# Optimization experiments

Measured on AMD Instinct MI355X. Metric: run time of the kernel, lower is better.

The kernel has to match this reference:

```python
import jax, jax.numpy as jnp
import numpy as np

N, E, D, DFF, OUT = 50000, 800000, 128, 256, 119
NUM_MASK = 7500

def setup_inputs() -> dict:
    key = jax.random.key(0)
    ks = jax.random.split(key, 12)
    return {
        "x": jax.random.normal(ks[0], (N, D), jnp.float32),
        "edge_index": jax.random.randint(ks[1], (2, E), 0, N, jnp.int64),
        "edge_attr": jax.random.randint(ks[2], (E, 2), 0, 3, jnp.int64),
        "masked_idx": jax.random.randint(ks[3], (NUM_MASK,), 0, N, jnp.int64),
        "prelu_a": jnp.float32(0.25),
        "W_enc": jax.random.normal(ks[4], (D, D), jnp.float32) * (1.0 / np.sqrt(D)),
        "emb1": jax.random.normal(ks[5], (6, D), jnp.float32) * 0.1,
        "emb2": jax.random.normal(ks[6], (3, D), jnp.float32) * 0.1,
        "W1": jax.random.normal(ks[7], (DFF, D), jnp.float32) * (1.0 / np.sqrt(D)),
        "b1": jnp.zeros((DFF,), jnp.float32),
        "W2": jax.random.normal(ks[8], (OUT, DFF), jnp.float32) * (1.0 / np.sqrt(DFF)),
        "b2": jnp.zeros((OUT,), jnp.float32),
    }

def reference(x, edge_index, edge_attr, masked_idx, prelu_a, W_enc, emb1, emb2, W1, b1, W2, b2):
    n = x.shape[0]
    # PReLU -> enc_to_dec (no bias) -> zero masked nodes
    h = jnp.where(x > 0, x, prelu_a * x)
    h = h @ W_enc.T
    h = h.at[masked_idx].set(0.0)
    # add self loops (self-loop edge_attr = [4, 0])
    loop = jnp.arange(n, dtype=edge_index.dtype)
    src = jnp.concatenate([edge_index[0], loop])
    dst = jnp.concatenate([edge_index[1], loop])
    et = jnp.concatenate([edge_attr[:, 0], jnp.full((n,), 4, edge_attr.dtype)])
    ed = jnp.concatenate([edge_attr[:, 1], jnp.zeros((n,), edge_attr.dtype)])
    edge_emb = emb1[et] + emb2[ed]          # [E+N, D]
    msg = h[src] + edge_emb                 # gather + add
    aggr = jax.ops.segment_sum(msg, dst, num_segments=n)  # scatter-add
    # GIN MLP update
    hid = jax.nn.relu(aggr @ W1.T + b1)
    return hid @ W2.T + b2
```

## Files before the change

kernel.cpp:

```cpp
#include <hip/hip_runtime.h>
#include <hip/hip_fp16.h>


typedef unsigned long long ull;
typedef _Float16 half8 __attribute__((ext_vector_type(8)));
typedef float    f32x4 __attribute__((ext_vector_type(4)));

#define MFMA16(a, b, c) __builtin_amdgcn_mfma_f32_16x16x32_f16(a, b, c, 0, 0, 0)
#define BCAP 4608
#define EPB  2048

__global__ __launch_bounds__(256) void k_wconv(const float* __restrict__ Wen,
                                               const float* __restrict__ W1,
                                               const float* __restrict__ W2,
                                               const float* __restrict__ b1,
                                               const float* __restrict__ emb1,
                                               const float* __restrict__ emb2,
                                               __half* __restrict__ Wc16,
                                               __half* __restrict__ W2_16p,
                                               float* __restrict__ tabs,
                                               int* __restrict__ gcur,
                                               int* __restrict__ off,
                                               int n, int E)
{
    int b = blockIdx.x, t = threadIdx.x;
    if (b < 128) {
        __shared__ float We[128 * 128];
        for (int i = t; i < 4096; i += 256) {
            int j = i >> 5, k4 = (i & 31) << 2;
            *(float4*)(We + (j << 7) + k4) = *(const float4*)(Wen + (j << 7) + k4);
        }
        __syncthreads();
        int r = (b << 1) | (t >> 7);
        int k = t & 127;
        const float* w1r = W1 + ((size_t)r << 7);
        float acc = 0.f;
#pragma unroll 8
        for (int j = 0; j < 128; ++j)
            acc = fmaf(w1r[j], We[(j << 7) + k], acc);
        Wc16[(r << 7) + k] = __float2half(acc);
    } else if (b < 192) {
#pragma unroll
        for (int u = 0; u < 2; ++u) {
            int i = (b - 128) * 512 + u * 256 + t;
            int r = i >> 8;
            W2_16p[i] = (r < 119) ? __float2half(W2[i]) : __half(0.0f);
        }
    } else if (b == 192) {
        int col = t;
        const float* w1r = W1 + ((size_t)col << 7);
        float s = 0.f, t0 = 0.f, t1 = 0.f, t2 = 0.f,
              u0 = 0.f, u1 = 0.f, u2 = 0.f;
        for (int j = 0; j < 128; ++j) {
            float w = w1r[j];
            s  = fmaf(emb1[512 + j] + emb2[j], w, s);
            t0 = fmaf(emb1[j],        w, t0);
            t1 = fmaf(emb1[128 + j],  w, t1);
            t2 = fmaf(emb1[256 + j],  w, t2);
            u0 = fmaf(emb2[j],        w, u0);
            u1 = fmaf(emb2[128 + j],  w, u1);
            u2 = fmaf(emb2[256 + j],  w, u2);
        }
        tabs[col]            = s + b1[col];
        tabs[256 + col]      = t0;
        tabs[512 + col]      = t1;
        tabs[768 + col]      = t2;
        tabs[1024 + col]     = u0;
        tabs[1280 + col]     = u1;
        tabs[1536 + col]     = u2;
    } else {
        gcur[t] = 0;
        if (t == 0) off[n] = E;
    }
}

__global__ __launch_bounds__(256) void k_pre(const float* __restrict__ x,
                                             const float* __restrict__ prelu_a,
                                             uint2* __restrict__ px16u2,
                                             const int* __restrict__ ei,
                                             const int* __restrict__ ea,
                                             int* __restrict__ gcur,
                                             unsigned int* __restrict__ binned,
                                             int n, int E, int nbPx, int nbBin)
{
    __shared__ int lcnt[256];
    int t = threadIdx.x;

    if ((int)blockIdx.x >= nbPx) {
        int b = blockIdx.x - nbPx;
        int e0 = b * EPB;
        lcnt[t] = 0;
        __syncthreads();
        unsigned int rec[8];
        int bk[8];
#pragma unroll
        for (int u = 0; u < 8; ++u) {
            int e = e0 + u * 256 + t;
            if (e < E) {
                int src = ei[e];
                int dst = ei[E + e];
                int et  = ea[2 * e];
                int ed  = ea[2 * e + 1];
                rec[u] = (unsigned int)src | ((unsigned int)et << 17)
                       | ((unsigned int)ed << 19)
                       | ((unsigned int)(dst & 255) << 21);
                bk[u] = dst >> 8;
                atomicAdd(&lcnt[bk[u]], 1);
            } else bk[u] = -1;
        }
        __syncthreads();
        int c = lcnt[t];
        lcnt[t] = (c > 0) ? atomicAdd(&gcur[t], c) : 0;
        __syncthreads();
#pragma unroll
        for (int u = 0; u < 8; ++u) {
            if (bk[u] >= 0) {
                int pos = atomicAdd(&lcnt[bk[u]], 1);
                if (pos < BCAP) binned[(size_t)bk[u] * BCAP + pos] = rec[u];
            }
        }
        return;
    }

    int idx = blockIdx.x * 256 + t;
    if (idx < n * 32) {
        float a = prelu_a[0];
        float4 v = *(const float4*)((const float*)x + (size_t)idx * 4);
        v.x = v.x > 0.f ? v.x : a * v.x;
        v.y = v.y > 0.f ? v.y : a * v.y;
        v.z = v.z > 0.f ? v.z : a * v.z;
        v.w = v.w > 0.f ? v.w : a * v.w;
        __half2 lo = __floats2half2_rn(v.x, v.y);
        __half2 hi = __floats2half2_rn(v.z, v.w);
        uint2 o;
        o.x = *(unsigned int*)&lo;
        o.y = *(unsigned int*)&hi;
        px16u2[idx] = o;
    }
}

__global__ void k_mask(const int* __restrict__ midx,
                       unsigned int* __restrict__ px16u, int nm)
{
    int idx = blockIdx.x * blockDim.x + threadIdx.x;
    if (idx >= nm * 64) return;
    int m = idx >> 6, l = idx & 63;
    px16u[(((size_t)midx[m]) << 6) + l] = 0u;
}

__global__ __launch_bounds__(256) void k_bucket(const unsigned int* __restrict__ binned,
                                                const int* __restrict__ gcur,
                                                ull* __restrict__ cnt64,
                                                int* __restrict__ off,
                                                int* __restrict__ sorted,
                                                int n, int nb)
{
    __shared__ ull lc[256];
    __shared__ int sg[2][256];
    __shared__ int curs[256];
    int b = blockIdx.x >> 1, half = blockIdx.x & 1;
    int t = threadIdx.x;

    int gv = (t < nb) ? min(gcur[t], BCAP) : 0;
    sg[0][t] = gv;
    lc[t] = 0;
    __syncthreads();
    int cb = 0;
    for (int d = 1; d < 256; d <<= 1) {
        int v = sg[cb][t];
        if (t >= d) v += sg[cb][t - d];
        sg[cb ^ 1][t] = v;
        cb ^= 1;
        __syncthreads();
    }
    int ebase = (b == 0) ? 0 : sg[cb][b - 1];
    int mcnt = min(gcur[b], BCAP);
    __syncthreads();

    const unsigned int* bp = binned + (size_t)b * BCAP;
    for (int i = t; i < mcnt; i += 256) {
        unsigned int rec = bp[i];
        int dl = (rec >> 21) & 255;
        int et = (rec >> 17) & 3;
        int ed = (rec >> 19) & 3;
        atomicAdd(&lc[dl], (1ULL << (10 * et)) | (1ULL << (30 + 10 * ed)));
    }
    __syncthreads();

    ull c = lc[t];
    int deg = (int)((c & 1023) + ((c >> 10) & 1023) + ((c >> 20) & 1023));
    sg[0][t] = deg;
    __syncthreads();
    cb = 0;
    for (int d = 1; d < 256; d <<= 1) {
        int v = sg[cb][t];
        if (t >= d) v += sg[cb][t - d];
        sg[cb ^ 1][t] = v;
        cb ^= 1;
        __syncthreads();
    }
    int loc = sg[cb][t] - deg;
    int dst = (b << 8) + t;
    if (dst < n && (t >> 7) == half) {
        cnt64[dst] = c;
        off[dst]   = ebase + loc;
    }
    curs[t] = ebase + loc;
    __syncthreads();

    for (int i = t; i < mcnt; i += 256) {
        unsigned int rec = bp[i];
        int dl = (rec >> 21) & 255;
        if ((dl >> 7) != half) continue;
        int p = atomicAdd(&curs[dl], 1);
        sorted[p] = (int)(rec & 0x1FFFF);
    }
}

__global__ __launch_bounds__(256) void k_agg(const uint2* __restrict__ px2,
                                             const int* __restrict__ off,
                                             const int* __restrict__ sorted,
                                             uint2* __restrict__ agg2, int n)
{
    int t = threadIdx.x;
    int l32 = t & 31;
    int node = blockIdx.x * 8 + (t >> 5);
    if (node >= n) return;

    uint2 hv = px2[(size_t)node * 32 + l32];
    float2 hA = __half22float2(*(__half2*)&hv.x);
    float2 hB = __half22float2(*(__half2*)&hv.y);
    float4 base = make_float4(hA.x, hA.y, hB.x, hB.y);

    __half2 aL[4], aH[4];
#pragma unroll
    for (int u = 0; u < 4; ++u) { aL[u] = __half2(); aH[u] = __half2(); }
    int i = off[node], e = off[node + 1];
    for (; i + 3 < e; i += 4) {
        int s0 = sorted[i],     s1 = sorted[i + 1];
        int s2 = sorted[i + 2], s3 = sorted[i + 3];
        uint2 v0 = px2[(size_t)s0 * 32 + l32];
        uint2 v1 = px2[(size_t)s1 * 32 + l32];
        uint2 v2 = px2[(size_t)s2 * 32 + l32];
        uint2 v3 = px2[(size_t)s3 * 32 + l32];
        aL[0] = __hadd2(aL[0], *(__half2*)&v0.x);
        aH[0] = __hadd2(aH[0], *(__half2*)&v0.y);
        aL[1] = __hadd2(aL[1], *(__half2*)&v1.x);
        aH[1] = __hadd2(aH[1], *(__half2*)&v1.y);
        aL[2] = __hadd2(aL[2], *(__half2*)&v2.x);
        aH[2] = __hadd2(aH[2], *(__half2*)&v2.y);
        aL[3] = __hadd2(aL[3], *(__half2*)&v3.x);
        aH[3] = __hadd2(aH[3], *(__half2*)&v3.y);
    }
    for (; i < e; ++i) {
        uint2 v0 = px2[(size_t)sorted[i] * 32 + l32];
        aL[0] = __hadd2(aL[0], *(__half2*)&v0.x);
        aH[0] = __hadd2(aH[0], *(__half2*)&v0.y);
    }
#pragma unroll
    for (int u = 0; u < 4; ++u) {
        float2 fL = __half22float2(aL[u]);
        float2 fH = __half22float2(aH[u]);
        base.x += fL.x; base.y += fL.y;
        base.z += fH.x; base.w += fH.y;
    }
    __half2 oL = __floats2half2_rn(base.x, base.y);
    __half2 oH = __floats2half2_rn(base.z, base.w);
    uint2 o;
    o.x = *(unsigned int*)&oL;
    o.y = *(unsigned int*)&oH;
    agg2[(size_t)node * 32 + l32] = o;
}

__global__ __launch_bounds__(256, 2) void k_mlp1(const __half* __restrict__ agg16,
                                                 const __half* __restrict__ Wc16,
                                                 const float* __restrict__ tabs,
                                                 const ull* __restrict__ cnt64,
                                                 __half* __restrict__ hid16, int n)
{
    __shared__ __half Wl[256 * 136];
    __shared__ float tl[7 * 256];
    int t = threadIdx.x;
    for (int c = t; c < 4096; c += 256) {
        int row = c >> 4, slot = c & 15;
        *(uint4*)((char*)Wl + row * 272 + slot * 16) =
            *(const uint4*)((const char*)Wc16 + (size_t)c * 16);
    }
    for (int c = t; c < 1792; c += 256) tl[c] = tabs[c];
    __syncthreads();
    int lane = t & 63, wid = t >> 6;
    int rowbase = blockIdx.x * 128 + wid * 32;
    int mr0 = min(rowbase + (lane & 15), n - 1);
    int mr1 = min(rowbase + 16 + (lane & 15), n - 1);
    int kg = (lane >> 4) * 8, slotb = lane >> 4;
    f32x4 acc[32] = {};
#pragma unroll
    for (int ks = 0; ks < 4; ++ks) {
        half8 a0 = *(const half8*)(agg16 + ((size_t)mr0 << 7) + ks * 32 + kg);
        half8 a1 = *(const half8*)(agg16 + ((size_t)mr1 << 7) + ks * 32 + kg);
        const char* wp = (const char*)Wl + (size_t)(lane & 15) * 272
                       + (ks * 4 + slotb) * 16;
#pragma unroll
        for (int ct = 0; ct < 16; ++ct) {
            half8 bf = *(const half8*)(wp + ct * (16 * 272));
            acc[ct * 2]     = MFMA16(a0, bf, acc[ct * 2]);
            acc[ct * 2 + 1] = MFMA16(a1, bf, acc[ct * 2 + 1]);
        }
    }
#pragma unroll
    for (int h = 0; h < 2; ++h) {
        float cf[4][6];
        int nodes[4];
#pragma unroll
        for (int r = 0; r < 4; ++r) {
            int node = rowbase + h * 16 + ((lane >> 4) << 2) + r;
            nodes[r] = node;
            ull c = (node < n) ? cnt64[node] : 0ULL;
            cf[r][0] = (float)(c & 1023);
            cf[r][1] = (float)((c >> 10) & 1023);
            cf[r][2] = (float)((c >> 20) & 1023);
            cf[r][3] = (float)((c >> 30) & 1023);
            cf[r][4] = (float)((c >> 40) & 1023);
            cf[r][5] = (float)((c >> 50) & 1023);
        }
#pragma unroll
        for (int ct = 0; ct < 16; ++ct) {
            int col = (ct << 4) + (lane & 15);
            float S  = tl[col];
            float T0 = tl[256 + col],  T1 = tl[512 + col],  T2 = tl[768 + col];
            float U0 = tl[1024 + col], U1 = tl[1280 + col], U2 = tl[1536 + col];
#pragma unroll
            for (int r = 0; r < 4; ++r) {
                if (nodes[r] < n) {
                    float v = acc[ct * 2 + h][r] + S;
                    v = fmaf(cf[r][0], T0, v);
                    v = fmaf(cf[r][1], T1, v);
                    v = fmaf(cf[r][2], T2, v);
                    v = fmaf(cf[r][3], U0, v);
                    v = fmaf(cf[r][4], U1, v);
                    v = fmaf(cf[r][5], U2, v);
                    hid16[((size_t)nodes[r] << 8) + col] =
                        __float2half(v > 0.f ? v : 0.f);
                }
            }
        }
    }
}

__global__ __launch_bounds__(256) void k_mlp2(const __half* __restrict__ hid16,
                                              const __half* __restrict__ W2_16p,
                                              const float* __restrict__ b2,
                                              float* __restrict__ out, int n)
{
    __shared__ __half W2l[128 * 264];
    int t = threadIdx.x;
    for (int c = t; c < 4096; c += 256) {
        int row = c >> 5, slot = c & 31;
        *(uint4*)((char*)W2l + row * 528 + slot * 16) =
            *(const uint4*)((const char*)W2_16p + (size_t)c * 16);
    }
    __syncthreads();
    int lane = t & 63, wid = t >> 6;
    int rowbase = blockIdx.x * 128 + wid * 32;
    int mr0 = min(rowbase + (lane & 15), n - 1);
    int mr1 = min(rowbase + 16 + (lane & 15), n - 1);
    int kg = (lane >> 4) * 8, slotb = lane >> 4;
    f32x4 acc[16] = {};
#pragma unroll
    for (int ks = 0; ks < 8; ++ks) {
        half8 a0 = *(const half8*)(hid16 + ((size_t)mr0 << 8) + ks * 32 + kg);
        half8 a1 = *(const half8*)(hid16 + ((size_t)mr1 << 8) + ks * 32 + kg);
        const char* wp = (const char*)W2l + (size_t)(lane & 15) * 528
                       + (ks * 4 + slotb) * 16;
#pragma unroll
        for (int ct = 0; ct < 8; ++ct) {
            half8 bf = *(const half8*)(wp + ct * (16 * 528));
            acc[ct * 2]     = MFMA16(a0, bf, acc[ct * 2]);
            acc[ct * 2 + 1] = MFMA16(a1, bf, acc[ct * 2 + 1]);
        }
    }
#pragma unroll
    for (int ct = 0; ct < 8; ++ct) {
        int col = (ct << 4) + (lane & 15);
        if (col >= 119) continue;
        float bb = b2[col];
#pragma unroll
        for (int h = 0; h < 2; ++h)
#pragma unroll
            for (int r = 0; r < 4; ++r) {
                int node = rowbase + h * 16 + ((lane >> 4) << 2) + r;
                if (node < n)
                    out[(size_t)node * 119 + col] = acc[ct * 2 + h][r] + bb;
            }
    }
}

extern "C" void kernel_launch(void* const* d_in, const int* in_sizes, int n_in,
                              void* d_out, int out_size, void* d_ws, size_t ws_size,
                              hipStream_t stream)
{
    const float* x    = (const float*)d_in[0];
    const int*   ei   = (const int*)d_in[1];
    const int*   ea   = (const int*)d_in[2];
    const int*   midx = (const int*)d_in[3];
    const float* pa   = (const float*)d_in[4];
    const float* Wen  = (const float*)d_in[5];
    const float* emb1 = (const float*)d_in[6];
    const float* emb2 = (const float*)d_in[7];
    const float* W1   = (const float*)d_in[8];
    const float* b1   = (const float*)d_in[9];
    const float* W2   = (const float*)d_in[10];
    const float* b2   = (const float*)d_in[11];
    float* out = (float*)d_out;

    int n  = in_sizes[0] / 128;
    int E  = in_sizes[1] / 2;
    int nm = in_sizes[3];
    int nb = (n + 255) >> 8;

    char* ws = (char*)d_ws;
    size_t HB = (size_t)n * 128 * 2;
    __half* agg16 = (__half*)ws;
    __half* px16  = (__half*)(ws + HB);
    __half* hid16 = (__half*)(ws + 2 * HB);
    char* p = ws + 4 * HB;
    __half* Wc16   = (__half*)p;  p += 256 * 128 * 2;
    __half* W2_16p = (__half*)p;  p += 128 * 256 * 2;
    float*  tabs   = (float*)p;   p += 7 * 256 * 4;
    ull* cnt64  = (ull*)p;        p += (size_t)n * 8;
    int* gcur   = (int*)p;        p += 256 * 4;
    int* off    = (int*)p;        p += (size_t)(n + 1) * 4;
    int* sorted = (int*)p;        p += (size_t)E * 4;
    unsigned int* binned = (unsigned int*)p;
    p += (size_t)nb * BCAP * 4;

    int nbPx  = (n * 32 + 255) / 256;
    int nbBin = (E + EPB - 1) / EPB;

    k_wconv<<<194, 256, 0, stream>>>(Wen, W1, W2, b1, emb1, emb2,
                                     Wc16, W2_16p, tabs, gcur, off, n, E);
    k_pre  <<<nbPx + nbBin, 256, 0, stream>>>(x, pa, (uint2*)px16, ei, ea,
                                              gcur, binned, n, E, nbPx, nbBin);
    k_mask <<<(nm * 64 + 255) / 256, 256, 0, stream>>>(midx, (unsigned int*)px16, nm);
    k_bucket<<<nb * 2, 256, 0, stream>>>(binned, gcur, cnt64, off, sorted, n, nb);
    k_agg  <<<(n + 7) / 8, 256, 0, stream>>>((const uint2*)px16, off, sorted,
                                             (uint2*)agg16, n);
    k_mlp1 <<<(n + 127) / 128, 256, 0, stream>>>(agg16, Wc16, tabs, cnt64,
                                                 hid16, n);
    k_mlp2 <<<(n + 127) / 128, 256, 0, stream>>>(hid16, W2_16p, b2, out, n);
}
```

Before: 125.5 us.

## Fuse MLP kernels via shared-memory hidden tile and fold masking into prep

Measured after the change: 144.3 us. +15.0%, slower.

```diff
diff --git a/kernel.cpp b/kernel.cpp
--- a/kernel.cpp
+++ b/kernel.cpp
@@ -16,12 +16,14 @@
                                                const float* __restrict__ b1,
                                                const float* __restrict__ emb1,
                                                const float* __restrict__ emb2,
+                                               const int* __restrict__ midx,
                                                __half* __restrict__ Wc16,
                                                __half* __restrict__ W2_16p,
                                                float* __restrict__ tabs,
                                                int* __restrict__ gcur,
                                                int* __restrict__ off,
-                                               int n, int E)
+                                               unsigned int* __restrict__ bm,
+                                               int n, int E, int nm)
 {
     int b = blockIdx.x, t = threadIdx.x;
     if (b < 128) {
@@ -71,11 +73,19 @@
     } else {
         gcur[t] = 0;
         if (t == 0) off[n] = E;
+        int nw = (n + 31) >> 5;
+        for (int i = t; i < nw; i += 256) bm[i] = 0u;
+        __syncthreads();
+        for (int m = t; m < nm; m += 256) {
+            int node = midx[m];
+            atomicOr(&bm[node >> 5], 1u << (node & 31));
+        }
     }
 }
 
 __global__ __launch_bounds__(256) void k_pre(const float* __restrict__ x,
                                              const float* __restrict__ prelu_a,
+                                             const unsigned int* __restrict__ bm,
                                              uint2* __restrict__ px16u2,
                                              const int* __restrict__ ei,
                                              const int* __restrict__ ea,
@@ -124,28 +134,24 @@
 
     int idx = blockIdx.x * 256 + t;
     if (idx < n * 32) {
+        int node = idx >> 5;
+        bool msk = (bm[node >> 5] >> (node & 31)) & 1u;
         float a = prelu_a[0];
         float4 v = *(const float4*)((const float*)x + (size_t)idx * 4);
         v.x = v.x > 0.f ? v.x : a * v.x;
         v.y = v.y > 0.f ? v.y : a * v.y;
         v.z = v.z > 0.f ? v.z : a * v.z;
         v.w = v.w > 0.f ? v.w : a * v.w;
-        __half2 lo = __floats2half2_rn(v.x, v.y);
-        __half2 hi = __floats2half2_rn(v.z, v.w);
         uint2 o;
-        o.x = *(unsigned int*)&lo;
-        o.y = *(unsigned int*)&hi;
+        if (msk) { o.x = 0u; o.y = 0u; }
+        else {
+            __half2 lo = __floats2half2_rn(v.x, v.y);
+            __half2 hi = __floats2half2_rn(v.z, v.w);
+            o.x = *(unsigned int*)&lo;
+            o.y = *(unsigned int*)&hi;
+        }
         px16u2[idx] = o;
     }
-}
-
-__global__ void k_mask(const int* __restrict__ midx,
-                       unsigned int* __restrict__ px16u, int nm)
-{
-    int idx = blockIdx.x * blockDim.x + threadIdx.x;
-    if (idx >= nm * 64) return;
-    int m = idx >> 6, l = idx & 63;
-    px16u[(((size_t)midx[m]) << 6) + l] = 0u;
 }
 
 __global__ __launch_bounds__(256) void k_bucket(const unsigned int* __restrict__ binned,
@@ -237,8 +243,10 @@
     for (int u = 0; u < 4; ++u) { aL[u] = __half2(); aH[u] = __half2(); }
     int i = off[node], e = off[node + 1];
     for (; i + 3 < e; i += 4) {
-        int s0 = sorted[i],     s1 = sorted[i + 1];
-        int s2 = sorted[i + 2], s3 = sorted[i + 3];
+        int s0 = __builtin_nontemporal_load(sorted + i);
+        int s1 = __builtin_nontemporal_load(sorted + i + 1);
+        int s2 = __builtin_nontemporal_load(sorted + i + 2);
+        int s3 = __builtin_nontemporal_load(sorted + i + 3);
         uint2 v0 = px2[(size_t)s0 * 32 + l32];
         uint2 v1 = px2[(size_t)s1 * 32 + l32];
         uint2 v2 = px2[(size_t)s2 * 32 + l32];
@@ -253,7 +261,8 @@
         aH[3] = __hadd2(aH[3], *(__half2*)&v3.y);
     }
     for (; i < e; ++i) {
-        uint2 v0 = px2[(size_t)sorted[i] * 32 + l32];
+        int s0 = __builtin_nontemporal_load(sorted + i);
+        uint2 v0 = px2[(size_t)s0 * 32 + l32];
         aL[0] = __hadd2(aL[0], *(__half2*)&v0.x);
         aH[0] = __hadd2(aH[0], *(__half2*)&v0.y);
     }
@@ -269,36 +278,41 @@
     uint2 o;
     o.x = *(unsigned int*)&oL;
     o.y = *(unsigned int*)&oH;
-    agg2[(size_t)node * 32 + l32] = o;
-}
-
-__global__ __launch_bounds__(256, 2) void k_mlp1(const __half* __restrict__ agg16,
-                                                 const __half* __restrict__ Wc16,
-                                                 const float* __restrict__ tabs,
-                                                 const ull* __restrict__ cnt64,
-                                                 __half* __restrict__ hid16, int n)
-{
-    __shared__ __half Wl[256 * 136];
+    __builtin_nontemporal_store(*(ull*)&o, (ull*)(agg2 + (size_t)node * 32 + l32));
+}
+
+__global__ __launch_bounds__(256) void k_mlp(const __half* __restrict__ agg16,
+                                             const __half* __restrict__ Wc16,
+                                             const float* __restrict__ tabs,
+                                             const ull* __restrict__ cnt64,
+                                             const __half* __restrict__ W2_16p,
+                                             const float* __restrict__ b2,
+                                             float* __restrict__ out, int n)
+{
+    __shared__ __half WA[256 * 136];
+    __shared__ __half HID[128 * 264];
     __shared__ float tl[7 * 256];
     int t = threadIdx.x;
     for (int c = t; c < 4096; c += 256) {
         int row = c >> 4, slot = c & 15;
-        *(uint4*)((char*)Wl + row * 272 + slot * 16) =
+        *(uint4*)((char*)WA + row * 272 + slot * 16) =
             *(const uint4*)((const char*)Wc16 + (size_t)c * 16);
     }
     for (int c = t; c < 1792; c += 256) tl[c] = tabs[c];
     __syncthreads();
+
     int lane = t & 63, wid = t >> 6;
     int rowbase = blockIdx.x * 128 + wid * 32;
     int mr0 = min(rowbase + (lane & 15), n - 1);
     int mr1 = min(rowbase + 16 + (lane & 15), n - 1);
     int kg = (lane >> 4) * 8, slotb = lane >> 4;
+
     f32x4 acc[32] = {};
 #pragma unroll
     for (int ks = 0; ks < 4; ++ks) {
         half8 a0 = *(const half8*)(agg16 + ((size_t)mr0 << 7) + ks * 32 + kg);
         half8 a1 = *(const half8*)(agg16 + ((size_t)mr1 << 7) + ks * 32 + kg);
-        const char* wp = (const char*)Wl + (size_t)(lane & 15) * 272
+        const char* wp = (const char*)WA + (size_t)(lane & 15) * 272
                        + (ks * 4 + slotb) * 16;
 #pragma unroll
         for (int ct = 0; ct < 16; ++ct) {
@@ -307,14 +321,20 @@
             acc[ct * 2 + 1] = MFMA16(a1, bf, acc[ct * 2 + 1]);
         }
     }
+    __syncthreads();
+
+    for (int c = t; c < 4096; c += 256) {
+        int row = c >> 5, slot = c & 31;
+        *(uint4*)((char*)WA + row * 528 + slot * 16) =
+            *(const uint4*)((const char*)W2_16p + (size_t)c * 16);
+    }
+
 #pragma unroll
     for (int h = 0; h < 2; ++h) {
         float cf[4][6];
-        int nodes[4];
 #pragma unroll
         for (int r = 0; r < 4; ++r) {
             int node = rowbase + h * 16 + ((lane >> 4) << 2) + r;
-            nodes[r] = node;
             ull c = (node < n) ? cnt64[node] : 0ULL;
             cf[r][0] = (float)(c & 1023);
             cf[r][1] = (float)((c >> 10) & 1023);
@@ -331,52 +351,33 @@
             float U0 = tl[1024 + col], U1 = tl[1280 + col], U2 = tl[1536 + col];
 #pragma unroll
             for (int r = 0; r < 4; ++r) {
-                if (nodes[r] < n) {
-                    float v = acc[ct * 2 + h][r] + S;
-                    v = fmaf(cf[r][0], T0, v);
-                    v = fmaf(cf[r][1], T1, v);
-                    v = fmaf(cf[r][2], T2, v);
-                    v = fmaf(cf[r][3], U0, v);
-                    v = fmaf(cf[r][4], U1, v);
-                    v = fmaf(cf[r][5], U2, v);
-                    hid16[((size_t)nodes[r] << 8) + col] =
-                        __float2half(v > 0.f ? v : 0.f);
-                }
+                int rowl = wid * 32 + h * 16 + ((lane >> 4) << 2) + r;
+                float v = acc[ct * 2 + h][r] + S;
+                v = fmaf(cf[r][0], T0, v);
+                v = fmaf(cf[r][1], T1, v);
+                v = fmaf(cf[r][2], T2, v);
+                v = fmaf(cf[r][3], U0, v);
+                v = fmaf(cf[r][4], U1, v);
+                v = fmaf(cf[r][5], U2, v);
+                HID[rowl * 264 + col] = __float2half(v > 0.f ? v : 0.f);
             }
         }
     }
-}
-
-__global__ __launch_bounds__(256) void k_mlp2(const __half* __restrict__ hid16,
-                                              const __half* __restrict__ W2_16p,
-                                              const float* __restrict__ b2,
-                                              float* __restrict__ out, int n)
-{
-    __shared__ __half W2l[128 * 264];
-    int t = threadIdx.x;
-    for (int c = t; c < 4096; c += 256) {
-        int row = c >> 5, slot = c & 31;
-        *(uint4*)((char*)W2l + row * 528 + slot * 16) =
-            *(const uint4*)((const char*)W2_16p + (size_t)c * 16);
-    }
-    __syncthreads();
-    int lane = t & 63, wid = t >> 6;
-    int rowbase = blockIdx.x * 128 + wid * 32;
-    int mr0 = min(rowbase + (lane & 15), n - 1);
-    int mr1 = min(rowbase + 16 + (lane & 15), n - 1);
-    int kg = (lane >> 4) * 8, slotb = lane >> 4;
-    f32x4 acc[16] = {};
+    __syncthreads();
+
+    f32x4 acc2[16] = {};
+    const char* hb0 = (const char*)HID + (size_t)(wid * 32 + (lane & 15)) * 528;
 #pragma unroll
     for (int ks = 0; ks < 8; ++ks) {
-        half8 a0 = *(const half8*)(hid16 + ((size_t)mr0 << 8) + ks * 32 + kg);
-        half8 a1 = *(const half8*)(hid16 + ((size_t)mr1 << 8) + ks * 32 + kg);
-        const char* wp = (const char*)W2l + (size_t)(lane & 15) * 528
+        half8 a0 = *(const half8*)(hb0 + (ks * 32 + kg) * 2);
+        half8 a1 = *(const half8*)(hb0 + 16 * 528 + (ks * 32 + kg) * 2);
+        const char* wp = (const char*)WA + (size_t)(lane & 15) * 528
                        + (ks * 4 + slotb) * 16;
 #pragma unroll
         for (int ct = 0; ct < 8; ++ct) {
             half8 bf = *(const half8*)(wp + ct * (16 * 528));
-            acc[ct * 2]     = MFMA16(a0, bf, acc[ct * 2]);
-            acc[ct * 2 + 1] = MFMA16(a1, bf, acc[ct * 2 + 1]);
+            acc2[ct * 2]     = MFMA16(a0, bf, acc2[ct * 2]);
+            acc2[ct * 2 + 1] = MFMA16(a1, bf, acc2[ct * 2 + 1]);
         }
     }
 #pragma unroll
@@ -390,7 +391,7 @@
             for (int r = 0; r < 4; ++r) {
                 int node = rowbase + h * 16 + ((lane >> 4) << 2) + r;
                 if (node < n)
-                    out[(size_t)node * 119 + col] = acc[ct * 2 + h][r] + bb;
+                    out[(size_t)node * 119 + col] = acc2[ct * 2 + h][r] + bb;
             }
     }
 }
@@ -422,13 +423,13 @@
     size_t HB = (size_t)n * 128 * 2;
     __half* agg16 = (__half*)ws;
     __half* px16  = (__half*)(ws + HB);
-    __half* hid16 = (__half*)(ws + 2 * HB);
-    char* p = ws + 4 * HB;
+    char* p = ws + 2 * HB;
     __half* Wc16   = (__half*)p;  p += 256 * 128 * 2;
     __half* W2_16p = (__half*)p;  p += 128 * 256 * 2;
     float*  tabs   = (float*)p;   p += 7 * 256 * 4;
     ull* cnt64  = (ull*)p;        p += (size_t)n * 8;
     int* gcur   = (int*)p;        p += 256 * 4;
+    unsigned int* bm = (unsigned int*)p;  p += 2048 * 4;
     int* off    = (int*)p;        p += (size_t)(n + 1) * 4;
     int* sorted = (int*)p;        p += (size_t)E * 4;
     unsigned int* binned = (unsigned int*)p;
@@ -437,15 +438,14 @@
     int nbPx  = (n * 32 + 255) / 256;
     int nbBin = (E + EPB - 1) / EPB;
 
-    k_wconv<<<194, 256, 0, stream>>>(Wen, W1, W2, b1, emb1, emb2,
-                                     Wc16, W2_16p, tabs, gcur, off, n, E);
-    k_pre  <<<nbPx + nbBin, 256, 0, stream>>>(x, pa, (uint2*)px16, ei, ea,
+    k_wconv<<<194, 256, 0, stream>>>(Wen, W1, W2, b1, emb1, emb2, midx,
+                                     Wc16, W2_16p, tabs, gcur, off, bm,
+                                     n, E, nm);
+    k_pre  <<<nbPx + nbBin, 256, 0, stream>>>(x, pa, bm, (uint2*)px16, ei, ea,
                                               gcur, binned, n, E, nbPx, nbBin);
-    k_mask <<<(nm * 64 + 255) / 256, 256, 0, stream>>>(midx, (unsigned int*)px16, nm);
     k_bucket<<<nb * 2, 256, 0, stream>>>(binned, gcur, cnt64, off, sorted, n, nb);
     k_agg  <<<(n + 7) / 8, 256, 0, stream>>>((const uint2*)px16, off, sorted,
                                              (uint2*)agg16, n);
-    k_mlp1 <<<(n + 127) / 128, 256, 0, stream>>>(agg16, Wc16, tabs, cnt64,
-                                                 hid16, n);
-    k_mlp2 <<<(n + 127) / 128, 256, 0, stream>>>(hid16, W2_16p, b2, out, n);
-}
+    k_mlp  <<<(n + 127) / 128, 256, 0, stream>>>(agg16, Wc16, tabs, cnt64,
+                                                 W2_16p, b2, out, n);
+}
```
